# Performance work log

Hardware: AMD Instinct MI355X
Metric: run time of the kernel (lower is better)

Reference implementation:

```python
import jax, jax.numpy as jnp
import numpy as np

VOC, EMB, HID = 32000, 512, 1024
B, S = 16, 256


def setup_inputs() -> dict:
    key = jax.random.key(0)
    ks = jax.random.split(key, 12)
    s_e = 1.0 / np.sqrt(HID)
    inp = {
        "inputs": jax.random.randint(ks[0], (B, S), 0, VOC, dtype=jnp.int64),
        "emb": jax.random.normal(ks[1], (VOC, EMB), dtype=jnp.float32),
        "W_ih1": jax.random.uniform(ks[2], (4 * HID, EMB), minval=-s_e, maxval=s_e),
        "W_hh1": jax.random.uniform(ks[3], (4 * HID, HID), minval=-s_e, maxval=s_e),
        "b_ih1": jax.random.uniform(ks[4], (4 * HID,), minval=-s_e, maxval=s_e),
        "b_hh1": jax.random.uniform(ks[5], (4 * HID,), minval=-s_e, maxval=s_e),
        "W_ih2": jax.random.uniform(ks[6], (4 * HID, HID), minval=-s_e, maxval=s_e),
        "W_hh2": jax.random.uniform(ks[7], (4 * HID, HID), minval=-s_e, maxval=s_e),
        "b_ih2": jax.random.uniform(ks[8], (4 * HID,), minval=-s_e, maxval=s_e),
        "b_hh2": jax.random.uniform(ks[9], (4 * HID,), minval=-s_e, maxval=s_e),
        "W_log": jax.random.uniform(ks[10], (VOC, HID), minval=-s_e, maxval=s_e),
        "b_log": jnp.zeros((VOC,), dtype=jnp.float32),  # init_weights zeroes logits bias
    }
    return inp


def _lstm_cell(x, h, c, W_ih, W_hh, b_ih, b_hh):
    # PyTorch LSTMCell: gates ordered (i, f, g, o)
    g = x @ W_ih.T + b_ih + h @ W_hh.T + b_hh  # [B, 4H]
    i, f, gg, o = jnp.split(g, 4, axis=-1)
    c_new = jax.nn.sigmoid(f) * c + jax.nn.sigmoid(i) * jnp.tanh(gg)
    h_new = jax.nn.sigmoid(o) * jnp.tanh(c_new)
    return h_new, c_new


def reference(inputs, emb, W_ih1, W_hh1, b_ih1, b_hh1,
              W_ih2, W_hh2, b_ih2, b_hh2, W_log, b_log):
    # Dropout is evaluated in inference mode (identity), for determinism.
    embed = emb[inputs]  # [B, S, E]
    xs = jnp.swapaxes(embed, 0, 1)  # [S, B, E]
    bsz = inputs.shape[0]
    h1 = jnp.zeros((bsz, HID), embed.dtype)
    c1 = jnp.zeros((bsz, HID), embed.dtype)
    h2 = jnp.zeros((bsz, HID), embed.dtype)
    c2 = jnp.zeros((bsz, HID), embed.dtype)

    def step(carry, x_t):
        h1, c1, h2, c2 = carry
        h1, c1 = _lstm_cell(x_t, h1, c1, W_ih1, W_hh1, b_ih1, b_hh1)
        h2, c2 = _lstm_cell(h1, h2, c2, W_ih2, W_hh2, b_ih2, b_hh2)
        return (h1, c1, h2, c2), h2

    _, hid_seq = jax.lax.scan(step, (h1, c1, h2, c2), xs)  # [S, B, H]
    hid_seq = jnp.swapaxes(hid_seq, 0, 1)  # [B, S, H]
    logits = hid_seq @ W_log.T + b_log  # [B, S, V]
    return jax.nn.log_softmax(logits, axis=-1)
```

## Files before the change

kernel.cpp:

```cpp
#include <hip/hip_runtime.h>
#include <hip/hip_bf16.h>

typedef __attribute__((ext_vector_type(8))) _Float16 half8;
typedef __attribute__((ext_vector_type(4))) _Float16 half4;
typedef __attribute__((ext_vector_type(4))) float f32x4;
typedef __attribute__((ext_vector_type(4))) unsigned int u32x4;

#define VOC 32000
#define EMB 512
#define HID 1024
#define SS  256
#define NROW 4096
#define CHK 43
#define CSTRIDE 64
#define SLOTB (64 * CSTRIDE * 16)
#define NS 4
#define SPIN (1 << 16)
#define ROWH 264
#define NTILE (32 * 250)

__device__ __forceinline__ float sigf(float x) {
    return 1.f / (1.f + __expf(-x));
}
__device__ __forceinline__ float tanh_c(float x) {
    x = fminf(fmaxf(x, -15.f), 15.f);
    float e = __expf(2.f * x);
    return (e - 1.f) / (e + 1.f);
}

__device__ __forceinline__ u32x4 ldg_u4_cc(const void* p) {
    u32x4 r;
    asm volatile("global_load_dwordx4 %0, %1, off sc0 sc1" : "=v"(r) : "v"(p));
    return r;
}
__device__ __forceinline__ void stg_u4_cc(void* p, u32x4 v) {
    asm volatile("global_store_dwordx4 %0, %1, off sc0 sc1" :: "v"(p), "v"(v) : "memory");
}
__device__ __forceinline__ void stg_h8_cc(_Float16* p, half8 v) {
    asm volatile("global_store_dwordx4 %0, %1, off sc0 sc1" :: "v"(p), "v"(v) : "memory");
}
__device__ __forceinline__ void stg_u32_cc(unsigned* p, unsigned v) {
    asm volatile("global_store_dword %0, %1, off sc0 sc1" :: "v"(p), "v"(v) : "memory");
}
__device__ __forceinline__ unsigned ldg_u32_cc(const unsigned* p) {
    unsigned v;
    asm volatile("global_load_dword %0, %1, off sc0 sc1\n\ts_waitcnt vmcnt(0)"
                 : "=v"(v) : "v"(p) : "memory");
    return v;
}
__device__ __forceinline__ half8 to_agpr(half8 v) {
    asm volatile("" : "+a"(v));
    return v;
}
__device__ __forceinline__ void gload16(const void* g, void* lds) {
    __builtin_amdgcn_global_load_lds(
        (const __attribute__((address_space(1))) unsigned int*)(uintptr_t)g,
        (__attribute__((address_space(3))) unsigned int*)(unsigned int)(uintptr_t)lds,
        16, 0, 0);
}

__global__ void k_zero(float* p, int n) {
    int i = blockIdx.x * blockDim.x + threadIdx.x;
    int st = gridDim.x * blockDim.x;
    for (; i < n; i += st) p[i] = 0.f;
}

__global__ void k_cvt_all(const float* __restrict__ s0, const float* __restrict__ s1,
                          const float* __restrict__ s2, const float* __restrict__ s3,
                          const float* __restrict__ s4,
                          _Float16* __restrict__ d0, _Float16* __restrict__ d1,
                          _Float16* __restrict__ d2, _Float16* __restrict__ d3,
                          _Float16* __restrict__ d4) {
    const int n0 = 4096 * 512 / 4;
    const int n1 = 4096 * 1024 / 4;
    const int n4 = VOC * 1024 / 4;
    const int nT = n0 + 3 * n1 + n4;
    int i = blockIdx.x * 256 + threadIdx.x;
    int st = gridDim.x * 256;
    for (; i < nT; i += st) {
        const float* s; _Float16* d; int k = i;
        if (k < n0) { s = s0; d = d0; }
        else {
            k -= n0;
            if (k < n1) { s = s1; d = d1; }
            else {
                k -= n1;
                if (k < n1) { s = s2; d = d2; }
                else {
                    k -= n1;
                    if (k < n1) { s = s3; d = d3; }
                    else { k -= n1; s = s4; d = d4; }
                }
            }
        }
        float4 v = ((const float4*)s)[k];
        half4 o = {(_Float16)v.x, (_Float16)v.y, (_Float16)v.z, (_Float16)v.w};
        ((half4*)d)[k] = o;
    }
}

__global__ void k_bias(const float* bi1, const float* bh1,
                       const float* bi2, const float* bh2,
                       float* b1, float* b2) {
    int i = blockIdx.x * blockDim.x + threadIdx.x;
    if (i < 4 * HID) { b1[i] = bi1[i] + bh1[i]; b2[i] = bi2[i] + bh2[i]; }
}

__global__ void k_embed(const int* __restrict__ tok, const float* __restrict__ emb,
                        _Float16* __restrict__ A) {
    int idx = blockIdx.x * 256 + threadIdx.x;
    if (idx >= NROW * (EMB / 4)) return;
    int r = idx >> 7, c4 = idx & 127;
    int t = r >> 4, b = r & 15;
    int token = tok[b * SS + t];
    float4 v = ((const float4*)(emb + (size_t)token * EMB))[c4];
    half4 o = {(_Float16)v.x, (_Float16)v.y, (_Float16)v.z, (_Float16)v.w};
    ((half4*)(A + (size_t)r * EMB))[c4] = o;
}

template <int F16OUT>
__global__ __launch_bounds__(512, 1) void k_gemm8(
    const _Float16* __restrict__ A, const _Float16* __restrict__ B,
    const float* __restrict__ bias, float* __restrict__ Cf,
    _Float16* __restrict__ Ch, int M, int N, int K, int scatter,
    int rowOff, int colOff) {
    __shared__ __align__(16) char smem[131072];
    int tid = threadIdx.x;
    int wave = tid >> 6, lane = tid & 63;
    int wm = wave >> 2, wn = wave & 3;
    int nbx = gridDim.x;
    int lin = blockIdx.y * nbx + blockIdx.x;
    {
        int n = nbx * gridDim.y;
        if ((n & 7) == 0) { int cpx = n >> 3; lin = (lin & 7) * cpx + (lin >> 3); }
    }
    int bRow = rowOff + (lin / nbx) * 256, bCol = colOff + (lin % nbx) * 256;
    int nt = K >> 6;
    int lrow = lane & 15, kq = lane >> 4;

    auto stage = [&](int mat, int h, int t) {
        const _Float16* src = mat ? B : A;
        int r0 = mat ? bCol : bRow;
        char* dst = smem + (size_t)(t & 1) * 65536 + mat * 32768 + h * 16384;
#pragma unroll
        for (int j = 0; j < 2; ++j) {
            int ci = j * 512 + tid;
            int row = ci >> 3, slot = ci & 7;
            int grow = h * 128 + row;
            int gsl = slot ^ (row & 7);
            gload16(src + (size_t)(r0 + grow) * K + t * 64 + gsl * 8, dst + ci * 16);
        }
    };
    auto rdA = [&](int bf, int mi, int kk) -> half8 {
        int r = wm * 128 + mi * 16 + lrow;
        int sl = (kk * 4 + kq) ^ (lrow & 7);
        return *(const half8*)(smem + (size_t)bf * 65536 + r * 128 + sl * 16);
    };
    auto rdB = [&](int bf, int ni, int kk) -> half8 {
        int r = wn * 64 + ni * 16 + lrow;
        int sl = (kk * 4 + kq) ^ (lrow & 7);
        return *(const half8*)(smem + (size_t)bf * 65536 + 32768 + r * 128 + sl * 16);
    };

    f32x4 acc[8][4] = {};

    stage(1, 0, 0); stage(0, 0, 0); stage(1, 1, 0); stage(0, 1, 0);
    if (nt > 1) { stage(1, 0, 1); stage(0, 0, 1); }

    for (int u = 0; u < nt; ++u) {
        int bf = u & 1;
        if (u + 1 == nt) asm volatile("s_waitcnt vmcnt(0)" ::: "memory");
        else             asm volatile("s_waitcnt vmcnt(4)" ::: "memory");
        __builtin_amdgcn_s_barrier();
        __builtin_amdgcn_sched_barrier(0);
        if (u + 1 < nt) stage(1, 1, u + 1);
        half8 a[8][2], b[4][2];
#pragma unroll
        for (int mi = 0; mi < 8; ++mi)
#pragma unroll
            for (int kk = 0; kk < 2; ++kk)
                a[mi][kk] = rdA(bf, mi, kk);
#pragma unroll
        for (int ni = 0; ni < 4; ++ni)
#pragma unroll
            for (int kk = 0; kk < 2; ++kk)
                b[ni][kk] = rdB(bf, ni, kk);
        __builtin_amdgcn_s_setprio(1);
#pragma unroll
        for (int mi = 0; mi < 8; ++mi)
#pragma unroll
            for (int ni = 0; ni < 4; ++ni) {
                acc[mi][ni] = __builtin_amdgcn_mfma_f32_16x16x32_f16(a[mi][0], b[ni][0], acc[mi][ni], 0, 0, 0);
                acc[mi][ni] = __builtin_amdgcn_mfma_f32_16x16x32_f16(a[mi][1], b[ni][1], acc[mi][ni], 0, 0, 0);
            }
        __builtin_amdgcn_s_setprio(0);
        asm volatile("s_waitcnt lgkmcnt(0)" ::: "memory");
        __builtin_amdgcn_s_barrier();
        __builtin_amdgcn_sched_barrier(0);
        if (u + 1 < nt) stage(0, 1, u + 1);
        if (u + 2 < nt) { stage(1, 0, u + 2); stage(0, 0, u + 2); }
    }

    float bv[4];
#pragma unroll
    for (int ni = 0; ni < 4; ++ni)
        bv[ni] = bias[bCol + wn * 64 + ni * 16 + lrow];
#pragma unroll
    for (int mi = 0; mi < 8; ++mi)
#pragma unroll
        for (int ni = 0; ni < 4; ++ni)
#pragma unroll
            for (int q = 0; q < 4; ++q) {
                int gr = bRow + wm * 128 + mi * 16 + kq * 4 + q;
                int gc = bCol + wn * 64 + ni * 16 + lrow;
                float v = acc[mi][ni][q] + bv[ni];
                size_t orow = scatter ? (size_t)(((gr & 15) << 8) | (gr >> 4)) : (size_t)gr;
                if (F16OUT) Ch[orow * (size_t)N + gc] = (_Float16)v;
                else        Cf[orow * (size_t)N + gc] = v;
            }
}

__device__ __forceinline__ void poll_stage2(const char* base, int exp, int cnt,
                                            unsigned short* hs, int sbp, int r) {
    u32x4 cv[11];
#pragma unroll
    for (int j = 0; j < 11; ++j)
        if (j < cnt) cv[j] = ldg_u4_cc(base + j * 64);
    for (int it = 0; it < SPIN; ++it) {
        asm volatile("s_waitcnt vmcnt(0)" ::: "memory");
        __builtin_amdgcn_sched_barrier(0);
        bool bad = false;
#pragma unroll
        for (int j = 0; j < 11; ++j)
            if (j < cnt && (int)cv[j][3] < exp) {
                cv[j] = ldg_u4_cc(base + j * 64);
                bad = true;
            }
        if (!bad) break;
        __builtin_amdgcn_s_sleep(1);
    }
#pragma unroll
    for (int j = 0; j < 11; ++j)
        if (j < cnt) {
            int c = r + 4 * j;
            unsigned* dst = (unsigned*)((char*)hs + sbp * (2 * ROWH) + c * 12);
            dst[0] = cv[j][0]; dst[1] = cv[j][1]; dst[2] = cv[j][2];
        }
}

__device__ __forceinline__ void gemm_ws(
    const _Float16* __restrict__ h2seq, const _Float16* __restrict__ Wlog,
    const float* __restrict__ blog, _Float16* __restrict__ logh,
    unsigned* prog2, unsigned* wq, char* smem, int tid) {
    int wave = tid >> 6, lane = tid & 63;
    int wr = (wave >> 1) * 64, wc = (wave & 1) * 64;
    int lrow = lane & 15, kq = lane >> 4;
    int lrow4 = (lane >> 4) * 4;
    volatile int* tsh = (int*)(smem + 84960);
    int pcg = -1;
    for (;;) {
        __syncthreads();
        if (tid == 0) *tsh = (int)atomicAdd(wq, 1u);
        __syncthreads();
        int idx = *tsh;
        if (idx >= NTILE) break;
        int tr = idx / 250, tc = idx - tr * 250;
        int needed = tr * 8 + 8;
        if (pcg < needed) {
            if (tid < 64) {
                const unsigned* pp = prog2 + (size_t)tid * 16;
                for (int it = 0; it < SPIN; ++it) {
                    unsigned v = ldg_u32_cc(pp);
                    if ((int)v >= needed) break;
                    __builtin_amdgcn_s_sleep(16);
                }
            }
            __syncthreads();
            pcg = needed;
        }
        int bRow = tr * 128, bCol = tc * 128;
        auto stage = [&](int u) {
            int bf = u & 1;
#pragma unroll
            for (int j = 0; j < 2; ++j) {
                int ci = j * 256 + tid;
                int row = ci >> 2, sl = ci & 3;
                int gsl = (sl ^ (row & 3)) * 8;
                char* basep = smem + bf * 16384 + (j * 256 + wave * 64) * 16;
                gload16(h2seq + (size_t)(bRow + row) * HID + u * 32 + gsl, basep);
                gload16(Wlog + (size_t)(bCol + row) * HID + u * 32 + gsl,
                        basep + 8192);
            }
        };
        auto rdA = [&](int bf, int i) -> half8 {
            int r = wr + 16 * i + lrow;
            int p = kq ^ (r & 3);
            return *(const half8*)(smem + bf * 16384 + r * 64 + p * 16);
        };
        auto rdB = [&](int bf, int j) -> half8 {
            int r = wc + 16 * j + lrow;
            int p = kq ^ (r & 3);
            return *(const half8*)(smem + bf * 16384 + 8192 + r * 64 + p * 16);
        };
        f32x4 acc[4][4] = {};
        stage(0);
        for (int u = 0; u < 32; ++u) {
            if (u + 1 < 32) {
                stage(u + 1);
                asm volatile("s_waitcnt vmcnt(4)" ::: "memory");
            } else {
                asm volatile("s_waitcnt vmcnt(0)" ::: "memory");
            }
            __builtin_amdgcn_s_barrier();
            __builtin_amdgcn_sched_barrier(0);
            int bf = u & 1;
            half8 a[4], b[4];
#pragma unroll
            for (int i = 0; i < 4; ++i) a[i] = rdA(bf, i);
#pragma unroll
            for (int j = 0; j < 4; ++j) b[j] = rdB(bf, j);
            __builtin_amdgcn_s_setprio(1);
#pragma unroll
            for (int i = 0; i < 4; ++i)
#pragma unroll
                for (int j = 0; j < 4; ++j)
                    acc[i][j] = __builtin_amdgcn_mfma_f32_16x16x32_f16(a[i], b[j], acc[i][j], 0, 0, 0);
            __builtin_amdgcn_s_setprio(0);
            asm volatile("s_waitcnt lgkmcnt(0)" ::: "memory");
            __builtin_amdgcn_s_barrier();
            __builtin_amdgcn_sched_barrier(0);
        }
#pragma unroll
        for (int i = 0; i < 4; ++i)
#pragma unroll
            for (int j = 0; j < 4; ++j)
#pragma unroll
                for (int q = 0; q < 4; ++q) {
                    int gr = bRow + wr + 16 * i + lrow4 + q;
                    int gc = bCol + wc + 16 * j + lrow;
                    size_t orow = (size_t)(((gr & 15) << 8) | (gr >> 4));
                    logh[orow * (size_t)VOC + gc] = (_Float16)(acc[i][j][q] + blog[gc]);
                }
    }
}

__global__ __launch_bounds__(256, 1) void k_fused(
    const _Float16* __restrict__ X,
    const _Float16* __restrict__ Whh1, const _Float16* __restrict__ Wih2,
    const _Float16* __restrict__ Whh2, const float* __restrict__ b2s,
    char* __restrict__ h1buf, char* __restrict__ h2buf,
    unsigned* __restrict__ prog, _Float16* __restrict__ h2seq,
    const _Float16* __restrict__ Wlog, const float* __restrict__ blog,
    _Float16* __restrict__ logh) {
    __shared__ __align__(16) char smem[84992];
    int tid = threadIdx.x;
    int bid = blockIdx.x;
    unsigned* prog2 = prog + 2048;
    unsigned* wq = prog + 3072;

    if (bid >= 128) {
        gemm_ws(h2seq, Wlog, blog, logh, prog2, wq, smem, tid);
        return;
    }

    unsigned short* hsPA = (unsigned short*)smem;
    unsigned short* hsPB = (unsigned short*)(smem + 33792);
    float* gsp = (float*)(smem + 67584);
    unsigned short* hstage = (unsigned short*)(smem + 83968);
    int w = tid >> 6, l = tid & 63;
    int layer = bid >> 6, sb = bid & 63;
    int sbp = tid >> 2, r = tid & 3;
    int cnt = (r == 3) ? 10 : 11;
    size_t choff = (size_t)(sbp * CSTRIDE + r) * 16;
    int hp = l >> 5;
    int hoff = (l & 15) * 16 + ((l >> 4) & 1) * 8;

    half8 wA[32];
    half8 wB[32];
    {
        const _Float16* base = layer ? Wih2 : Whh1;
        const _Float16* wp = base + (size_t)(w * HID + sb * 16 + (l & 15)) * HID + (l >> 4) * 8;
#pragma unroll
        for (int kt = 0; kt < 32; ++kt)
            wA[kt] = to_agpr(*(const half8*)(wp + kt * 32));
        if (layer) {
            const _Float16* wq2 = Whh2 + (size_t)(w * HID + sb * 16 + (l & 15)) * HID + (l >> 4) * 8;
#pragma unroll
            for (int kt = 0; kt < 32; ++kt)
                wB[kt] = to_agpr(*(const half8*)(wq2 + kt * 32));
        }
    }
    float bias_v = layer ? b2s[w * HID + sb * 16 + (l & 15)] : 0.f;

    int eb = tid >> 4, ecol = tid & 15;
    int gidx = ((eb >> 2) * 16 + ecol) * 4 + (eb & 3);
    float creg = 0.f;
    int pc = 0;

    if (!layer) {
        const _Float16* xbase = X + (size_t)w * HID + sb * 16 + (l & 15);
        int bq = (l >> 4) * 4;
        f32x4 xreg;
        {
            const _Float16* xp = xbase + (size_t)bq * 4096;
            xreg[0] = (float)xp[0]; xreg[1] = (float)xp[4096];
            xreg[2] = (float)xp[8192]; xreg[3] = (float)xp[12288];
        }
        for (int g = 0; g < SS; ++g) {
            int tn = (g + 1 < SS) ? g + 1 : SS - 1;
            const _Float16* xp = xbase + (size_t)(tn * 16 + bq) * 4096;
            float xn0 = (float)xp[0], xn1 = (float)xp[4096],
                  xn2 = (float)xp[8192], xn3 = (float)xp[12288];

            poll_stage2(h1buf + ((g - 1) & 3) * SLOTB + choff, g, cnt, hsPA, sbp, r);
            __syncthreads();
            if (tid == 0) stg_u32_cc(prog + (size_t)bid * 16, (unsigned)(g + 1));

            f32x4 a0 = xreg, a1 = {}, a2 = {}, a3 = {};
#pragma unroll
            for (int c = 0; c < 4; ++c) {
                half8 ha[8];
#pragma unroll
                for (int j = 0; j < 8; ++j)
                    ha[j] = *(const half8*)(hsPA + (2 * (c * 8 + j) + hp) * ROWH + hoff);
#pragma unroll
                for (int j = 0; j < 8; ++j) {
                    f32x4* ac = (j & 3) == 0 ? &a0 : (j & 3) == 1 ? &a1 : (j & 3) == 2 ? &a2 : &a3;
                    *ac = __builtin_amdgcn_mfma_f32_16x16x32_f16(ha[j], wA[c * 8 + j], *ac, 0, 0, 0);
                }
            }
            a0 = (a0 + a1) + (a2 + a3);

            *(f32x4*)(&gsp[w * 1024 + l * 4]) = a0;
            __syncthreads();

            float gi = gsp[gidx], gf = gsp[1024 + gidx],
                  gg = gsp[2048 + gidx], go = gsp[3072 + gidx];
            float cn = sigf(gf) * creg + sigf(gi) * tanh_c(gg);
            float hn = sigf(go) * tanh_c(cn);
            creg = cn;
            _Float16 hh = (_Float16)hn;
            unsigned short hu;
            __builtin_memcpy(&hu, &hh, 2);
            hstage[eb * 16 + ecol] = hu;
            xreg[0] = xn0; xreg[1] = xn1; xreg[2] = xn2; xreg[3] = xn3;
            __syncthreads();

            if (tid < 128 && pc < g - 2) {
                const unsigned* pp = prog + (size_t)tid * 16;
                for (int it = 0; it < SPIN; ++it) {
                    unsigned v = ldg_u32_cc(pp);
                    if ((int)v >= g - 2) { pc = (int)v; break; }
                    __builtin_amdgcn_s_sleep(1);
                }
            }
            __syncthreads();
            if (w == 0 && l < CHK) {
                const unsigned* hsu = (const unsigned*)hstage;
                u32x4 pv;
                pv[0] = hsu[l * 3]; pv[1] = hsu[l * 3 + 1]; pv[2] = hsu[l * 3 + 2];
                pv[3] = (unsigned)(g + 1);
                stg_u4_cc(h1buf + (g & 3) * SLOTB + (size_t)(sb * CSTRIDE + l) * 16, pv);
            }
        }
    } else {
        for (int s = 0; s < SS; ++s) {
            poll_stage2(h2buf + ((s - 1) & 3) * SLOTB + choff, s, cnt, hsPB, sbp, r);
            poll_stage2(h1buf + (s & 3) * SLOTB + choff, s + 1, cnt, hsPA, sbp, r);
            __syncthreads();
            if (tid == 0) stg_u32_cc(prog + (size_t)bid * 16, (unsigned)(s + 1));
            if (tid == 1) stg_u32_cc(prog + 2048 + (size_t)sb * 16, (unsigned)s);

            f32x4 a0 = {bias_v, bias_v, bias_v, bias_v}, a1 = {}, a2 = {}, a3 = {};
#pragma unroll
            for (int c = 0; c < 4; ++c) {
                half8 ha[8];
#pragma unroll
                for (int j = 0; j < 8; ++j)
                    ha[j] = *(const half8*)(hsPB + (2 * (c * 8 + j) + hp) * ROWH + hoff);
#pragma unroll
                for (int j = 0; j < 8; ++j) {
                    f32x4* ac = (j & 3) == 0 ? &a0 : (j & 3) == 1 ? &a1 : (j & 3) == 2 ? &a2 : &a3;
                    *ac = __builtin_amdgcn_mfma_f32_16x16x32_f16(ha[j], wB[c * 8 + j], *ac, 0, 0, 0);
                }
            }
#pragma unroll
            for (int c = 0; c < 4; ++c) {
                half8 ha[8];
#pragma unroll
                for (int j = 0; j < 8; ++j)
                    ha[j] = *(const half8*)(hsPA + (2 * (c * 8 + j) + hp) * ROWH + hoff);
#pragma unroll
                for (int j = 0; j < 8; ++j) {
                    f32x4* ac = (j & 3) == 0 ? &a0 : (j & 3) == 1 ? &a1 : (j & 3) == 2 ? &a2 : &a3;
                    *ac = __builtin_amdgcn_mfma_f32_16x16x32_f16(ha[j], wA[c * 8 + j], *ac, 0, 0, 0);
                }
            }
            a0 = (a0 + a1) + (a2 + a3);

            *(f32x4*)(&gsp[w * 1024 + l * 4]) = a0;
            __syncthreads();

            float gi = gsp[gidx], gf = gsp[1024 + gidx],
                  gg = gsp[2048 + gidx], go = gsp[3072 + gidx];
            float cn = sigf(gf) * creg + sigf(gi) * tanh_c(gg);
            float hn = sigf(go) * tanh_c(cn);
            creg = cn;
            _Float16 hh = (_Float16)hn;
            unsigned short hu;
            __builtin_memcpy(&hu, &hh, 2);
            hstage[eb * 16 + ecol] = hu;
            __syncthreads();

            if (tid < 64 && pc < s - 2) {
                const unsigned* pp = prog + (size_t)(64 + tid) * 16;
                for (int it = 0; it < SPIN; ++it) {
                    unsigned v = ldg_u32_cc(pp);
                    if ((int)v >= s - 2) { pc = (int)v; break; }
                    __builtin_amdgcn_s_sleep(1);
                }
            }
            __syncthreads();
            if (w == 0 && l < CHK) {
                const unsigned* hsu = (const unsigned*)hstage;
                u32x4 pv;
                pv[0] = hsu[l * 3]; pv[1] = hsu[l * 3 + 1]; pv[2] = hsu[l * 3 + 2];
                pv[3] = (unsigned)(s + 1);
                stg_u4_cc(h2buf + (s & 3) * SLOTB + (size_t)(sb * CSTRIDE + l) * 16, pv);
            }
            if (w == 1 && l < 32) {
                half8 hv = *(const half8*)((const char*)hstage + l * 16);
                stg_h8_cc(h2seq + (size_t)(s * 16 + (l >> 1)) * HID + sb * 16 + (l & 1) * 8, hv);
            }
        }
        asm volatile("s_waitcnt vmcnt(0)" ::: "memory");
        __syncthreads();
        if (tid == 0) stg_u32_cc(prog + 2048 + (size_t)sb * 16, 256u);
    }

    if (logh) {
        __syncthreads();
        gemm_ws(h2seq, Wlog, blog, logh, prog2, wq, smem, tid);
    }
}

__global__ __launch_bounds__(320) void k_lsm_f(float* __restrict__ logits) {
    int r = blockIdx.x, tid = threadIdx.x;
    float* row = logits + (size_t)r * VOC;
    f32x4 v[25];
    float m = -3.4e38f;
#pragma unroll
    for (int j = 0; j < 25; ++j) {
        v[j] = ((const f32x4*)row)[tid + 320 * j];
        m = fmaxf(fmaxf(fmaxf(m, v[j][0]), fmaxf(v[j][1], v[j][2])), v[j][3]);
    }
#pragma unroll
    for (int off = 1; off < 64; off <<= 1) m = fmaxf(m, __shfl_xor(m, off));
    __shared__ float sm[5], ssum[5];
    int wv = tid >> 6;
    if ((tid & 63) == 0) sm[wv] = m;
    __syncthreads();
    m = fmaxf(fmaxf(fmaxf(sm[0], sm[1]), fmaxf(sm[2], sm[3])), sm[4]);
    float s = 0.f;
#pragma unroll
    for (int j = 0; j < 25; ++j)
        s += (__expf(v[j][0] - m) + __expf(v[j][1] - m)) +
             (__expf(v[j][2] - m) + __expf(v[j][3] - m));
#pragma unroll
    for (int off = 1; off < 64; off <<= 1) s += __shfl_xor(s, off);
    if ((tid & 63) == 0) ssum[wv] = s;
    __syncthreads();
    s = (ssum[0] + ssum[1]) + (ssum[2] + ssum[3]) + ssum[4];
    float lse = m + __logf(s);
#pragma unroll
    for (int j = 0; j < 25; ++j) {
        f32x4 o = v[j];
        o[0] -= lse; o[1] -= lse; o[2] -= lse; o[3] -= lse;
        ((f32x4*)row)[tid + 320 * j] = o;
    }
}

__global__ __launch_bounds__(320) void k_lsm_h(const _Float16* __restrict__ lg,
                                               float* __restrict__ out) {
    int r = blockIdx.x, tid = threadIdx.x;
    const half4* row = (const half4*)(lg + (size_t)r * VOC);
    float* orow = out + (size_t)r * VOC;
    half4 v[25];
    float m = -3.4e38f;
#pragma unroll
    for (int j = 0; j < 25; ++j) {
        v[j] = row[tid + 320 * j];
        float a = (float)v[j][0], b = (float)v[j][1], c = (float)v[j][2], d = (float)v[j][3];
        m = fmaxf(fmaxf(fmaxf(m, a), fmaxf(b, c)), d);
    }
#pragma unroll
    for (int off = 1; off < 64; off <<= 1) m = fmaxf(m, __shfl_xor(m, off));
    __shared__ float sm[5], ssum[5];
    int wv = tid >> 6;
    if ((tid & 63) == 0) sm[wv] = m;
    __syncthreads();
    m = fmaxf(fmaxf(fmaxf(sm[0], sm[1]), fmaxf(sm[2], sm[3])), sm[4]);
    float s = 0.f;
#pragma unroll
    for (int j = 0; j < 25; ++j)
        s += (__expf((float)v[j][0] - m) + __expf((float)v[j][1] - m)) +
             (__expf((float)v[j][2] - m) + __expf((float)v[j][3] - m));
#pragma unroll
    for (int off = 1; off < 64; off <<= 1) s += __shfl_xor(s, off);
    if ((tid & 63) == 0) ssum[wv] = s;
    __syncthreads();
    s = (ssum[0] + ssum[1]) + (ssum[2] + ssum[3]) + ssum[4];
    float lse = m + __logf(s);
#pragma unroll
    for (int j = 0; j < 25; ++j) {
        f32x4 o = {(float)v[j][0] - lse, (float)v[j][1] - lse,
                   (float)v[j][2] - lse, (float)v[j][3] - lse};
        ((f32x4*)orow)[tid + 320 * j] = o;
    }
}

extern "C" void kernel_launch(void* const* d_in, const int* in_sizes, int n_in,
                              void* d_out, int out_size, void* d_ws, size_t ws_size,
                              hipStream_t stream) {
    const int*   tok   = (const int*)d_in[0];
    const float* emb   = (const float*)d_in[1];
    const float* W_ih1 = (const float*)d_in[2];
    const float* W_hh1 = (const float*)d_in[3];
    const float* b_ih1 = (const float*)d_in[4];
    const float* b_hh1 = (const float*)d_in[5];
    const float* W_ih2 = (const float*)d_in[6];
    const float* W_hh2 = (const float*)d_in[7];
    const float* b_ih2 = (const float*)d_in[8];
    const float* b_hh2 = (const float*)d_in[9];
    const float* W_log = (const float*)d_in[10];
    const float* b_log = (const float*)d_in[11];
    float* out = (float*)d_out;

    char* w = (char*)d_ws;
    auto alloc = [&](size_t bytes) {
        char* p = w;
        w += (bytes + 255) & ~(size_t)255;
        return p;
    };
    _Float16* Wih1h = (_Float16*)alloc((size_t)4096 * 512 * 2);
    _Float16* Whh1h = (_Float16*)alloc((size_t)4096 * 1024 * 2);
    _Float16* Wih2h = (_Float16*)alloc((size_t)4096 * 1024 * 2);
    _Float16* Whh2h = (_Float16*)alloc((size_t)4096 * 1024 * 2);
    _Float16* Wlogh = (_Float16*)alloc((size_t)VOC * 1024 * 2);
    _Float16* Abuf  = (_Float16*)alloc((size_t)4096 * 512 * 2);
    _Float16* Xh    = (_Float16*)alloc((size_t)4096 * 4096 * 2);
    _Float16* h2seq = (_Float16*)alloc((size_t)4096 * 1024 * 2);
    float* b1s      = (float*)alloc(4096 * 4);
    float* b2s      = (float*)alloc(4096 * 4);
    char* h1buf     = alloc(NS * SLOTB);
    char* h2buf     = alloc(NS * SLOTB);
    unsigned* prog  = (unsigned*)alloc(12544);
    size_t need = (size_t)(w - (char*)d_ws) + (size_t)NROW * VOC * 2;
    _Float16* logh = (need <= ws_size) ? (_Float16*)alloc((size_t)NROW * VOC * 2) : nullptr;

    k_zero<<<64, 256, 0, stream>>>((float*)h1buf, (2 * NS * SLOTB + 12544) / 4);

    k_cvt_all<<<2048, 256, 0, stream>>>(W_ih1, W_hh1, W_ih2, W_hh2, W_log,
                                        Wih1h, Whh1h, Wih2h, Whh2h, Wlogh);
    k_bias<<<16, 256, 0, stream>>>(b_ih1, b_hh1, b_ih2, b_hh2, b1s, b2s);

    k_embed<<<2048, 256, 0, stream>>>(tok, emb, Abuf);
    k_gemm8<1><<<dim3(16, 16), 512, 0, stream>>>(Abuf, Wih1h, b1s, nullptr, Xh,
                                                 4096, 4096, 512, 0, 0, 0);

    if (logh) {
        k_fused<<<256, 256, 0, stream>>>(Xh, Whh1h, Wih2h, Whh2h, b2s,
                                         h1buf, h2buf, prog, h2seq,
                                         Wlogh, b_log, logh);
        k_lsm_h<<<4096, 320, 0, stream>>>(logh, out);
    } else {
        k_fused<<<128, 256, 0, stream>>>(Xh, Whh1h, Wih2h, Whh2h, b2s,
                                         h1buf, h2buf, prog, h2seq,
                                         Wlogh, b_log, nullptr);
        k_gemm8<0><<<dim3(VOC / 256, 16), 512, 0, stream>>>(h2seq, Wlogh, b_log,
                                                            out, nullptr,
                                                            4096, VOC, 1024, 1, 0, 0);
        k_lsm_f<<<4096, 320, 0, stream>>>(out);
    }
}
```

Baseline: 1.417 ms.

## Widen logits GEMM K-tile to 64 and prefetch two stages ahead

The logits GEMM tile loop now stages 64-wide K slices instead of 32, using a 32KB double buffer with an 8-way XOR swizzle. Each tile is consumed in two MFMA sub-steps, so the loop runs 16 iterations instead of 32. Loads are issued two iterations ahead instead of one, with vmcnt(8) waits. The aim is to halve the barrier count and hide more global-load latency, at the cost of twice the LDS footprint.

```diff
diff --git a/kernel.cpp b/kernel.cpp
--- a/kernel.cpp
+++ b/kernel.cpp
@@ -282,53 +282,51 @@
         auto stage = [&](int u) {
             int bf = u & 1;
 #pragma unroll
-            for (int j = 0; j < 2; ++j) {
+            for (int j = 0; j < 4; ++j) {
                 int ci = j * 256 + tid;
-                int row = ci >> 2, sl = ci & 3;
-                int gsl = (sl ^ (row & 3)) * 8;
-                char* basep = smem + bf * 16384 + (j * 256 + wave * 64) * 16;
-                gload16(h2seq + (size_t)(bRow + row) * HID + u * 32 + gsl, basep);
-                gload16(Wlog + (size_t)(bCol + row) * HID + u * 32 + gsl,
-                        basep + 8192);
-            }
-        };
-        auto rdA = [&](int bf, int i) -> half8 {
-            int r = wr + 16 * i + lrow;
-            int p = kq ^ (r & 3);
-            return *(const half8*)(smem + bf * 16384 + r * 64 + p * 16);
-        };
-        auto rdB = [&](int bf, int j) -> half8 {
-            int r = wc + 16 * j + lrow;
-            int p = kq ^ (r & 3);
-            return *(const half8*)(smem + bf * 16384 + 8192 + r * 64 + p * 16);
+                int row = ci >> 3, sl = ci & 7;
+                int gsl = sl ^ (row & 7);
+                char* db = smem + bf * 32768 + (j * 256 + wave * 64) * 16;
+                gload16(h2seq + (size_t)(bRow + row) * HID + u * 64 + gsl * 8, db);
+                gload16(Wlog + (size_t)(bCol + row) * HID + u * 64 + gsl * 8, db + 16384);
+            }
         };
         f32x4 acc[4][4] = {};
         stage(0);
-        for (int u = 0; u < 32; ++u) {
-            if (u + 1 < 32) {
-                stage(u + 1);
-                asm volatile("s_waitcnt vmcnt(4)" ::: "memory");
-            } else {
-                asm volatile("s_waitcnt vmcnt(0)" ::: "memory");
-            }
+        stage(1);
+        for (int u = 0; u < 16; ++u) {
+            int bf = u & 1;
+            if (u + 1 < 16) asm volatile("s_waitcnt vmcnt(8)" ::: "memory");
+            else            asm volatile("s_waitcnt vmcnt(0)" ::: "memory");
             __builtin_amdgcn_s_barrier();
             __builtin_amdgcn_sched_barrier(0);
-            int bf = u & 1;
-            half8 a[4], b[4];
-#pragma unroll
-            for (int i = 0; i < 4; ++i) a[i] = rdA(bf, i);
-#pragma unroll
-            for (int j = 0; j < 4; ++j) b[j] = rdB(bf, j);
-            __builtin_amdgcn_s_setprio(1);
-#pragma unroll
-            for (int i = 0; i < 4; ++i)
-#pragma unroll
-                for (int j = 0; j < 4; ++j)
-                    acc[i][j] = __builtin_amdgcn_mfma_f32_16x16x32_f16(a[i], b[j], acc[i][j], 0, 0, 0);
-            __builtin_amdgcn_s_setprio(0);
+#pragma unroll
+            for (int kk = 0; kk < 2; ++kk) {
+                half8 a[4], b[4];
+#pragma unroll
+                for (int i = 0; i < 4; ++i) {
+                    int r = wr + 16 * i + lrow;
+                    int sl = (kk * 4 + kq) ^ (r & 7);
+                    a[i] = *(const half8*)(smem + bf * 32768 + r * 128 + sl * 16);
+                }
+#pragma unroll
+                for (int j = 0; j < 4; ++j) {
+                    int r = wc + 16 * j + lrow;
+                    int sl = (kk * 4 + kq) ^ (r & 7);
+                    b[j] = *(const half8*)(smem + bf * 32768 + 16384 + r * 128 + sl * 16);
+                }
+                __builtin_amdgcn_s_setprio(1);
+#pragma unroll
+                for (int i = 0; i < 4; ++i)
+#pragma unroll
+                    for (int j = 0; j < 4; ++j)
+                        acc[i][j] = __builtin_amdgcn_mfma_f32_16x16x32_f16(a[i], b[j], acc[i][j], 0, 0, 0);
+                __builtin_amdgcn_s_setprio(0);
+            }
             asm volatile("s_waitcnt lgkmcnt(0)" ::: "memory");
             __builtin_amdgcn_s_barrier();
             __builtin_amdgcn_sched_barrier(0);
+            if (u + 2 < 16) stage(u + 2);
         }
 #pragma unroll
         for (int i = 0; i < 4; ++i)
```

Result: no change. 1.423 ms (+0.4%).
